# Optimization experiments

Measured on AMD Instinct MI355X. Metric: run time of the kernel, lower is better.

The kernel has to match this reference:

```python
import jax, jax.numpy as jnp
import numpy as np

# Dims: a=1, b=8 (dispatch groups), m=256 (tokens per group), H=2048, E=8 experts,
# inter=1024 -> n = 2*inter = 2048 (fused gate+up projection width), K=2.
A, B, M, H, E, K, N = 1, 8, 256, 2048, 8, 2, 2048


def setup_inputs() -> dict:
    key = jax.random.key(0)
    k1, k2, k3 = jax.random.split(key, 3)
    hidden_4d = jax.random.normal(k1, (A, B, M, H), dtype=jnp.float32)
    sparsity = jax.random.uniform(k2, (A, B, K, E), dtype=jnp.float32)
    # learned parameter: nn.Parameter(torch.randn(1, E, H, inter*2) * 0.02)
    gate_up_proj = jax.random.normal(k3, (1, E, H, N), dtype=jnp.float32) * 0.02
    return {"hidden_4d": hidden_4d, "sparsity": sparsity, "gate_up_proj": gate_up_proj}


def reference(hidden_4d, sparsity, gate_up_proj):
    ib = gate_up_proj[0]              # [E, H, N]
    sp_mask = sparsity[:, :, 0, :]    # [A, B, E]
    # Original: out = einsum('abmk,ekn->abemn') * mask[..., None, None]; return out.sum()
    # Fused into a single contraction to a scalar (identical math, no abemn intermediate):
    # sum_{a,b,e,m,n} (sum_k h[a,b,m,k] * w[e,k,n]) * mask[a,b,e]
    per_en = jnp.einsum('abmk,ekn->aben', hidden_4d, ib)   # [A,B,E,N] (sum over m folded below)
    return jnp.einsum('aben,abe->', per_en, sp_mask)
```

## Files before the change

kernel.cpp:

```cpp
#include <hip/hip_runtime.h>

#define Bn 8
#define Mn 256
#define Hn 2048
#define En 8
#define Kn 2
#define Nn 2048


__global__ void reduce_kernel(const float* __restrict__ hidden,
                              const float* __restrict__ gup,
                              float* __restrict__ hs,
                              float* __restrict__ wsum) {
    const int bid = blockIdx.x;
    const int t   = threadIdx.x;
    if (bid < 4096) {
        const int wave = t >> 6;
        const int lane = t & 63;
        const int row  = bid * 4 + wave;
        const float4* p = (const float4*)(gup + (size_t)row * Nn);
        float acc = 0.f;
#pragma unroll
        for (int i = 0; i < 8; ++i) {
            float4 v = p[i * 64 + lane];
            acc += (v.x + v.y) + (v.z + v.w);
        }
#pragma unroll
        for (int off = 32; off > 0; off >>= 1)
            acc += __shfl_down(acc, off, 64);
        if (lane == 0) wsum[row] = acc;
    } else {
        const int bi = bid - 4096;
        const int mc = bi & 7;
        const int kt = (bi >> 3) & 7;
        const int b  = bi >> 6;
        const int k  = kt * 256 + t;
        const float* p = hidden + (size_t)b * Mn * Hn + (size_t)(mc * 32) * Hn + k;
        float acc = 0.f;
#pragma unroll
        for (int m = 0; m < 32; ++m)
            acc += p[(size_t)m * Hn];
        atomicAdd(&hs[b * Hn + k], acc);
    }
}

__global__ void final_kernel(const float* __restrict__ sparsity,
                             const float* __restrict__ hs,
                             const float* __restrict__ wsum,
                             float* __restrict__ out) {
    __shared__ float sp[Bn][En];
    __shared__ float red[4];
    const int t = threadIdx.x;
    if (t < Bn * En) {
        const int b = t >> 3, e = t & 7;
        sp[b][e] = sparsity[b * (Kn * En) + e];
    }
    __syncthreads();
    float acc = 0.f;
    for (int k = t; k < Hn; k += 256) {
        float h[Bn];
#pragma unroll
        for (int b = 0; b < Bn; ++b) h[b] = hs[b * Hn + k];
#pragma unroll
        for (int e = 0; e < En; ++e) {
            float g = 0.f;
#pragma unroll
            for (int b = 0; b < Bn; ++b) g += sp[b][e] * h[b];
            acc += wsum[e * Hn + k] * g;
        }
    }
#pragma unroll
    for (int off = 32; off > 0; off >>= 1)
        acc += __shfl_down(acc, off, 64);
    const int lane = t & 63, wave = t >> 6;
    if (lane == 0) red[wave] = acc;
    __syncthreads();
    if (t == 0) out[0] = red[0] + red[1] + red[2] + red[3];
}

extern "C" void kernel_launch(void* const* d_in, const int* in_sizes, int n_in,
                              void* d_out, int out_size, void* d_ws, size_t ws_size,
                              hipStream_t stream) {
    const float* hidden   = (const float*)d_in[0];
    const float* sparsity = (const float*)d_in[1];
    const float* gup      = (const float*)d_in[2];

    float* hs   = (float*)d_ws;
    float* wsum = hs + Bn * Hn;

    hipMemsetAsync(d_ws, 0, Bn * Hn * sizeof(float), stream);
    reduce_kernel<<<4096 + 512, 256, 0, stream>>>(hidden, gup, hs, wsum);
    final_kernel<<<1, 256, 0, stream>>>(sparsity, hs, wsum, (float*)d_out);
}
```

Baseline: 208.2 us.

## Replace atomic hidden reduction with float4 partials and drop memset

The hidden-state column reduction now uses float4 loads across 4 rows per thread group plus a shared-memory reduction, and writes per-chunk partial sums instead of doing atomicAdds. This removes the memset launch and the atomic traffic. The hidden blocks are reordered to come first, and the weight-sum loop loads all values up front for more memory-level parallelism. The final kernel grows to 1024 threads and sums the 8 partials per (b,k), which adds a little work to that single-block kernel.

```diff
diff --git a/kernel.cpp b/kernel.cpp
--- a/kernel.cpp
+++ b/kernel.cpp
@@ -10,46 +10,70 @@
 
 __global__ void reduce_kernel(const float* __restrict__ hidden,
                               const float* __restrict__ gup,
-                              float* __restrict__ hs,
+                              float* __restrict__ partial,
                               float* __restrict__ wsum) {
     const int bid = blockIdx.x;
     const int t   = threadIdx.x;
-    if (bid < 4096) {
+    if (bid < 1024) {
+        const int b  = bid >> 7;
+        const int mc = (bid >> 4) & 7;
+        const int kh = bid & 15;
+        const int col = t & 31;
+        const int tg  = t >> 5;
+        const int m0  = mc * 32 + tg * 4;
+        const float4* hp = (const float4*)(hidden + ((size_t)b * Mn + m0) * Hn + kh * 128);
+        float4 v0 = hp[0 * (Hn / 4) + col];
+        float4 v1 = hp[1 * (Hn / 4) + col];
+        float4 v2 = hp[2 * (Hn / 4) + col];
+        float4 v3 = hp[3 * (Hn / 4) + col];
+        float4 s;
+        s.x = (v0.x + v1.x) + (v2.x + v3.x);
+        s.y = (v0.y + v1.y) + (v2.y + v3.y);
+        s.z = (v0.z + v1.z) + (v2.z + v3.z);
+        s.w = (v0.w + v1.w) + (v2.w + v3.w);
+        __shared__ float4 sd[8][32];
+        sd[tg][col] = s;
+        __syncthreads();
+        if (t < 32) {
+            float4 r = sd[0][t];
+#pragma unroll
+            for (int g = 1; g < 8; ++g) {
+                float4 q = sd[g][t];
+                r.x += q.x; r.y += q.y; r.z += q.z; r.w += q.w;
+            }
+            ((float4*)partial)[(size_t)(b * 8 + mc) * (Hn / 4) + kh * 32 + t] = r;
+        }
+    } else {
         const int wave = t >> 6;
         const int lane = t & 63;
-        const int row  = bid * 4 + wave;
+        const int row  = (bid - 1024) * 4 + wave;
         const float4* p = (const float4*)(gup + (size_t)row * Nn);
-        float acc = 0.f;
-#pragma unroll
-        for (int i = 0; i < 8; ++i) {
-            float4 v = p[i * 64 + lane];
-            acc += (v.x + v.y) + (v.z + v.w);
-        }
+        float4 v0 = p[0 * 64 + lane];
+        float4 v1 = p[1 * 64 + lane];
+        float4 v2 = p[2 * 64 + lane];
+        float4 v3 = p[3 * 64 + lane];
+        float4 v4 = p[4 * 64 + lane];
+        float4 v5 = p[5 * 64 + lane];
+        float4 v6 = p[6 * 64 + lane];
+        float4 v7 = p[7 * 64 + lane];
+        float s01 = (v0.x + v0.y + v0.z + v0.w) + (v1.x + v1.y + v1.z + v1.w);
+        float s23 = (v2.x + v2.y + v2.z + v2.w) + (v3.x + v3.y + v3.z + v3.w);
+        float s45 = (v4.x + v4.y + v4.z + v4.w) + (v5.x + v5.y + v5.z + v5.w);
+        float s67 = (v6.x + v6.y + v6.z + v6.w) + (v7.x + v7.y + v7.z + v7.w);
+        float acc = (s01 + s23) + (s45 + s67);
 #pragma unroll
         for (int off = 32; off > 0; off >>= 1)
             acc += __shfl_down(acc, off, 64);
         if (lane == 0) wsum[row] = acc;
-    } else {
-        const int bi = bid - 4096;
-        const int mc = bi & 7;
-        const int kt = (bi >> 3) & 7;
-        const int b  = bi >> 6;
-        const int k  = kt * 256 + t;
-        const float* p = hidden + (size_t)b * Mn * Hn + (size_t)(mc * 32) * Hn + k;
-        float acc = 0.f;
-#pragma unroll
-        for (int m = 0; m < 32; ++m)
-            acc += p[(size_t)m * Hn];
-        atomicAdd(&hs[b * Hn + k], acc);
     }
 }
 
 __global__ void final_kernel(const float* __restrict__ sparsity,
-                             const float* __restrict__ hs,
+                             const float* __restrict__ partial,
                              const float* __restrict__ wsum,
                              float* __restrict__ out) {
     __shared__ float sp[Bn][En];
-    __shared__ float red[4];
+    __shared__ float red[16];
     const int t = threadIdx.x;
     if (t < Bn * En) {
         const int b = t >> 3, e = t & 7;
@@ -57,10 +81,16 @@
     }
     __syncthreads();
     float acc = 0.f;
-    for (int k = t; k < Hn; k += 256) {
+    for (int k = t; k < Hn; k += 1024) {
         float h[Bn];
 #pragma unroll
-        for (int b = 0; b < Bn; ++b) h[b] = hs[b * Hn + k];
+        for (int b = 0; b < Bn; ++b) {
+            float hb = 0.f;
+#pragma unroll
+            for (int mc = 0; mc < 8; ++mc)
+                hb += partial[(size_t)(b * 8 + mc) * Hn + k];
+            h[b] = hb;
+        }
 #pragma unroll
         for (int e = 0; e < En; ++e) {
             float g = 0.f;
@@ -75,7 +105,12 @@
     const int lane = t & 63, wave = t >> 6;
     if (lane == 0) red[wave] = acc;
     __syncthreads();
-    if (t == 0) out[0] = red[0] + red[1] + red[2] + red[3];
+    if (t == 0) {
+        float r = 0.f;
+#pragma unroll
+        for (int w = 0; w < 16; ++w) r += red[w];
+        out[0] = r;
+    }
 }
 
 extern "C" void kernel_launch(void* const* d_in, const int* in_sizes, int n_in,
@@ -85,10 +120,9 @@
     const float* sparsity = (const float*)d_in[1];
     const float* gup      = (const float*)d_in[2];
 
-    float* hs   = (float*)d_ws;
-    float* wsum = hs + Bn * Hn;
+    float* partial = (float*)d_ws;
+    float* wsum    = partial + Bn * 8 * Hn;
 
-    hipMemsetAsync(d_ws, 0, Bn * Hn * sizeof(float), stream);
-    reduce_kernel<<<4096 + 512, 256, 0, stream>>>(hidden, gup, hs, wsum);
-    final_kernel<<<1, 256, 0, stream>>>(sparsity, hs, wsum, (float*)d_out);
+    reduce_kernel<<<1024 + 4096, 256, 0, stream>>>(hidden, gup, partial, wsum);
+    final_kernel<<<1, 1024, 0, stream>>>(sparsity, partial, wsum, (float*)d_out);
 }
```

Result: slower. 214.5 us (+3.0%).

## Replace atomic hidden reduction with block-local float4 reduction and drop memset

Applied to the files above, without the earlier changes.

The hidden-sum part now has each block reduce a full 256-row column slice with float4 loads and a shared-memory tree, writing results directly instead of using atomicAdd. That removes the memset launch and the atomic traffic. The gate_up row-sum blocks now handle two rows per wave with all loads issued up front, which halves their block count and raises memory-level parallelism. The final kernel loop is fully unrolled. Having only 128 blocks on the hidden path may leave those blocks as the long tail.

```diff
diff --git a/kernel.cpp b/kernel.cpp
--- a/kernel.cpp
+++ b/kernel.cpp
@@ -14,33 +14,73 @@
                               float* __restrict__ wsum) {
     const int bid = blockIdx.x;
     const int t   = threadIdx.x;
-    if (bid < 4096) {
-        const int wave = t >> 6;
+    if (bid < 128) {
+        const int b   = bid >> 4;
+        const int kh  = bid & 15;
+        const int col = t & 31;
+        const int mg  = t >> 5;
+        const float4* hp = (const float4*)(hidden + ((size_t)b * Mn + mg * 32) * Hn)
+                           + kh * 32 + col;
+        float4 a0 = {0,0,0,0}, a1 = {0,0,0,0}, a2 = {0,0,0,0}, a3 = {0,0,0,0};
+#pragma unroll
+        for (int m = 0; m < 32; m += 4) {
+            float4 v0 = hp[(size_t)(m + 0) * (Hn / 4)];
+            float4 v1 = hp[(size_t)(m + 1) * (Hn / 4)];
+            float4 v2 = hp[(size_t)(m + 2) * (Hn / 4)];
+            float4 v3 = hp[(size_t)(m + 3) * (Hn / 4)];
+            a0.x += v0.x; a0.y += v0.y; a0.z += v0.z; a0.w += v0.w;
+            a1.x += v1.x; a1.y += v1.y; a1.z += v1.z; a1.w += v1.w;
+            a2.x += v2.x; a2.y += v2.y; a2.z += v2.z; a2.w += v2.w;
+            a3.x += v3.x; a3.y += v3.y; a3.z += v3.z; a3.w += v3.w;
+        }
+        float4 s;
+        s.x = (a0.x + a1.x) + (a2.x + a3.x);
+        s.y = (a0.y + a1.y) + (a2.y + a3.y);
+        s.z = (a0.z + a1.z) + (a2.z + a3.z);
+        s.w = (a0.w + a1.w) + (a2.w + a3.w);
+        __shared__ float4 sd[8][32];
+        sd[mg][col] = s;
+        __syncthreads();
+        if (t < 32) {
+            float4 r = sd[0][t];
+#pragma unroll
+            for (int g = 1; g < 8; ++g) {
+                float4 q = sd[g][t];
+                r.x += q.x; r.y += q.y; r.z += q.z; r.w += q.w;
+            }
+            ((float4*)hs)[(size_t)b * (Hn / 4) + kh * 32 + t] = r;
+        }
+    } else {
+        const int wave = (bid - 128) * 4 + (t >> 6);
         const int lane = t & 63;
-        const int row  = bid * 4 + wave;
-        const float4* p = (const float4*)(gup + (size_t)row * Nn);
-        float acc = 0.f;
+        const int r0 = wave * 2;
+        const float4* p0 = (const float4*)(gup + (size_t)r0 * Nn);
+        const float4* p1 = (const float4*)(gup + (size_t)(r0 + 1) * Nn);
+        float4 u0 = p0[0 * 64 + lane], u1 = p0[1 * 64 + lane];
+        float4 u2 = p0[2 * 64 + lane], u3 = p0[3 * 64 + lane];
+        float4 u4 = p0[4 * 64 + lane], u5 = p0[5 * 64 + lane];
+        float4 u6 = p0[6 * 64 + lane], u7 = p0[7 * 64 + lane];
+        float4 w0 = p1[0 * 64 + lane], w1 = p1[1 * 64 + lane];
+        float4 w2 = p1[2 * 64 + lane], w3 = p1[3 * 64 + lane];
+        float4 w4 = p1[4 * 64 + lane], w5 = p1[5 * 64 + lane];
+        float4 w6 = p1[6 * 64 + lane], w7 = p1[7 * 64 + lane];
+        float sa = ((u0.x + u0.y + u0.z + u0.w) + (u1.x + u1.y + u1.z + u1.w))
+                 + ((u2.x + u2.y + u2.z + u2.w) + (u3.x + u3.y + u3.z + u3.w))
+                 + ((u4.x + u4.y + u4.z + u4.w) + (u5.x + u5.y + u5.z + u5.w))
+                 + ((u6.x + u6.y + u6.z + u6.w) + (u7.x + u7.y + u7.z + u7.w));
+        float sb = ((w0.x + w0.y + w0.z + w0.w) + (w1.x + w1.y + w1.z + w1.w))
+                 + ((w2.x + w2.y + w2.z + w2.w) + (w3.x + w3.y + w3.z + w3.w))
+                 + ((w4.x + w4.y + w4.z + w4.w) + (w5.x + w5.y + w5.z + w5.w))
+                 + ((w6.x + w6.y + w6.z + w6.w) + (w7.x + w7.y + w7.z + w7.w));
 #pragma unroll
-        for (int i = 0; i < 8; ++i) {
-            float4 v = p[i * 64 + lane];
-            acc += (v.x + v.y) + (v.z + v.w);
+        for (int off = 32; off > 0; off >>= 1) {
+            sa += __shfl_down(sa, off, 64);
+            sb += __shfl_down(sb, off, 64);
         }
-#pragma unroll
-        for (int off = 32; off > 0; off >>= 1)
-            acc += __shfl_down(acc, off, 64);
-        if (lane == 0) wsum[row] = acc;
-    } else {
-        const int bi = bid - 4096;
-        const int mc = bi & 7;
-        const int kt = (bi >> 3) & 7;
-        const int b  = bi >> 6;
-        const int k  = kt * 256 + t;
-        const float* p = hidden + (size_t)b * Mn * Hn + (size_t)(mc * 32) * Hn + k;
-        float acc = 0.f;
-#pragma unroll
-        for (int m = 0; m < 32; ++m)
-            acc += p[(size_t)m * Hn];
-        atomicAdd(&hs[b * Hn + k], acc);
+        if (lane == 0) {
+            wsum[r0]     = sa;
+            wsum[r0 + 1] = sb;
+        }
     }
 }
 
@@ -57,7 +97,9 @@
     }
     __syncthreads();
     float acc = 0.f;
-    for (int k = t; k < Hn; k += 256) {
+#pragma unroll
+    for (int i = 0; i < Hn / 256; ++i) {
+        const int k = i * 256 + t;
         float h[Bn];
 #pragma unroll
         for (int b = 0; b < Bn; ++b) h[b] = hs[b * Hn + k];
@@ -75,7 +117,7 @@
     const int lane = t & 63, wave = t >> 6;
     if (lane == 0) red[wave] = acc;
     __syncthreads();
-    if (t == 0) out[0] = red[0] + red[1] + red[2] + red[3];
+    if (t == 0) out[0] = (red[0] + red[1]) + (red[2] + red[3]);
 }
 
 extern "C" void kernel_launch(void* const* d_in, const int* in_sizes, int n_in,
@@ -88,7 +130,6 @@
     float* hs   = (float*)d_ws;
     float* wsum = hs + Bn * Hn;
 
-    hipMemsetAsync(d_ws, 0, Bn * Hn * sizeof(float), stream);
-    reduce_kernel<<<4096 + 512, 256, 0, stream>>>(hidden, gup, hs, wsum);
+    reduce_kernel<<<128 + 2048, 256, 0, stream>>>(hidden, gup, hs, wsum);
     final_kernel<<<1, 256, 0, stream>>>(sparsity, hs, wsum, (float*)d_out);
 }
```

Measured after the change: 205.3 us. About the same (-1.4%).

## Replace atomic hidden reduction with in-block LDS reduce and drop memset

Applied to the files above, without the earlier changes.

The hidden-state column sums are now computed by 128 blocks that each cover a full batch and column slice, with vectorized nontemporal loads and an LDS cross-group reduction, so the atomicAdd path and the workspace memset launch are removed. The weight row-sum path now has each wave handle four rows, software-prefetching the next row's loads while reducing the current one, and writes the four results as one vector store. The final kernel loop is fully unrolled. This is meant to cut launch overhead and atomic traffic and to raise memory-level parallelism on a bandwidth-bound pass, at the cost of higher register pressure from the double-buffered loads.

```diff
diff --git a/kernel.cpp b/kernel.cpp
--- a/kernel.cpp
+++ b/kernel.cpp
@@ -7,6 +7,8 @@
 #define Kn 2
 #define Nn 2048
 
+typedef float vf4 __attribute__((ext_vector_type(4)));
+
 
 __global__ void reduce_kernel(const float* __restrict__ hidden,
                               const float* __restrict__ gup,
@@ -14,33 +16,66 @@
                               float* __restrict__ wsum) {
     const int bid = blockIdx.x;
     const int t   = threadIdx.x;
-    if (bid < 4096) {
-        const int wave = t >> 6;
+    if (bid < 128) {
+        const int b   = bid >> 4;
+        const int kh  = bid & 15;
+        const int col = t & 31;
+        const int mg  = t >> 5;
+        const vf4* hp = (const vf4*)(hidden + ((size_t)b * Mn + mg * 32) * Hn)
+                        + kh * 32 + col;
+        vf4 a0 = 0.f, a1 = 0.f, a2 = 0.f, a3 = 0.f;
+#pragma unroll
+        for (int m = 0; m < 32; m += 4) {
+            vf4 v0 = __builtin_nontemporal_load(hp + (size_t)(m + 0) * (Hn / 4));
+            vf4 v1 = __builtin_nontemporal_load(hp + (size_t)(m + 1) * (Hn / 4));
+            vf4 v2 = __builtin_nontemporal_load(hp + (size_t)(m + 2) * (Hn / 4));
+            vf4 v3 = __builtin_nontemporal_load(hp + (size_t)(m + 3) * (Hn / 4));
+            a0 += v0; a1 += v1; a2 += v2; a3 += v3;
+        }
+        vf4 s = (a0 + a1) + (a2 + a3);
+        __shared__ vf4 sd[8][32];
+        sd[mg][col] = s;
+        __syncthreads();
+        if (t < 32) {
+            vf4 r = sd[0][t];
+#pragma unroll
+            for (int g = 1; g < 8; ++g) r += sd[g][t];
+            ((vf4*)hs)[(size_t)b * (Hn / 4) + kh * 32 + t] = r;
+        }
+    } else {
+        const int wave = (bid - 128) * 4 + (t >> 6);
         const int lane = t & 63;
-        const int row  = bid * 4 + wave;
-        const float4* p = (const float4*)(gup + (size_t)row * Nn);
-        float acc = 0.f;
+        const size_t r0 = (size_t)wave * 4;
+        const vf4* base = (const vf4*)gup;
+        vf4 cur[8], nxt[8];
 #pragma unroll
-        for (int i = 0; i < 8; ++i) {
-            float4 v = p[i * 64 + lane];
-            acc += (v.x + v.y) + (v.z + v.w);
+        for (int i = 0; i < 8; ++i)
+            cur[i] = __builtin_nontemporal_load(base + r0 * 512 + i * 64 + lane);
+        float rowsum[4];
+#pragma unroll
+        for (int j = 0; j < 4; ++j) {
+            if (j < 3) {
+#pragma unroll
+                for (int i = 0; i < 8; ++i)
+                    nxt[i] = __builtin_nontemporal_load(
+                        base + (r0 + j + 1) * 512 + i * 64 + lane);
+            }
+            vf4 v = ((cur[0] + cur[1]) + (cur[2] + cur[3]))
+                  + ((cur[4] + cur[5]) + (cur[6] + cur[7]));
+            float s = (v.x + v.y) + (v.z + v.w);
+#pragma unroll
+            for (int off = 32; off > 0; off >>= 1)
+                s += __shfl_down(s, off, 64);
+            rowsum[j] = s;
+            if (j < 3) {
+#pragma unroll
+                for (int i = 0; i < 8; ++i) cur[i] = nxt[i];
+            }
         }
-#pragma unroll
-        for (int off = 32; off > 0; off >>= 1)
-            acc += __shfl_down(acc, off, 64);
-        if (lane == 0) wsum[row] = acc;
-    } else {
-        const int bi = bid - 4096;
-        const int mc = bi & 7;
-        const int kt = (bi >> 3) & 7;
-        const int b  = bi >> 6;
-        const int k  = kt * 256 + t;
-        const float* p = hidden + (size_t)b * Mn * Hn + (size_t)(mc * 32) * Hn + k;
-        float acc = 0.f;
-#pragma unroll
-        for (int m = 0; m < 32; ++m)
-            acc += p[(size_t)m * Hn];
-        atomicAdd(&hs[b * Hn + k], acc);
+        if (lane == 0) {
+            vf4 o = { rowsum[0], rowsum[1], rowsum[2], rowsum[3] };
+            ((vf4*)wsum)[wave] = o;
+        }
     }
 }
 
@@ -57,7 +92,9 @@
     }
     __syncthreads();
     float acc = 0.f;
-    for (int k = t; k < Hn; k += 256) {
+#pragma unroll
+    for (int i = 0; i < Hn / 256; ++i) {
+        const int k = i * 256 + t;
         float h[Bn];
 #pragma unroll
         for (int b = 0; b < Bn; ++b) h[b] = hs[b * Hn + k];
@@ -75,7 +112,7 @@
     const int lane = t & 63, wave = t >> 6;
     if (lane == 0) red[wave] = acc;
     __syncthreads();
-    if (t == 0) out[0] = red[0] + red[1] + red[2] + red[3];
+    if (t == 0) out[0] = (red[0] + red[1]) + (red[2] + red[3]);
 }
 
 extern "C" void kernel_launch(void* const* d_in, const int* in_sizes, int n_in,
@@ -88,7 +125,6 @@
     float* hs   = (float*)d_ws;
     float* wsum = hs + Bn * Hn;
 
-    hipMemsetAsync(d_ws, 0, Bn * Hn * sizeof(float), stream);
-    reduce_kernel<<<4096 + 512, 256, 0, stream>>>(hidden, gup, hs, wsum);
+    reduce_kernel<<<128 + 1024, 256, 0, stream>>>(hidden, gup, hs, wsum);
     final_kernel<<<1, 256, 0, stream>>>(sparsity, hs, wsum, (float*)d_out);
 }
```

Result: faster. 190.2 us (-8.7%).
